# Kernel optimization log

Measured on AMD Instinct MI355X. Metric: run time of the kernel, lower is better.

The kernel has to match this reference:

```python
import jax, jax.numpy as jnp
import numpy as np

D_MODEL = 1024
NUM_HEADS = 16
HEAD_DIM = D_MODEL // NUM_HEADS


def setup_inputs() -> dict:
    key = jax.random.key(0)
    ks = jax.random.split(key, 9)
    s = 1.0 / np.sqrt(D_MODEL)
    x = jax.random.normal(ks[0], (2, 2048, D_MODEL), dtype=jnp.float32)
    Wq = jax.random.normal(ks[1], (D_MODEL, D_MODEL), dtype=jnp.float32) * s
    bq = jnp.zeros((D_MODEL,), dtype=jnp.float32)
    Wk = jax.random.normal(ks[2], (D_MODEL, D_MODEL), dtype=jnp.float32) * s
    bk = jnp.zeros((D_MODEL,), dtype=jnp.float32)
    Wv = jax.random.normal(ks[3], (D_MODEL, D_MODEL), dtype=jnp.float32) * s
    bv = jnp.zeros((D_MODEL,), dtype=jnp.float32)
    Wo = jax.random.normal(ks[4], (D_MODEL, D_MODEL), dtype=jnp.float32) * s
    bo = jnp.zeros((D_MODEL,), dtype=jnp.float32)
    return {"x": x, "Wq": Wq, "bq": bq, "Wk": Wk, "bk": bk,
            "Wv": Wv, "bv": bv, "Wo": Wo, "bo": bo}


def reference(x, Wq, bq, Wk, bk, Wv, bv, Wo, bo):
    B, S, D = x.shape
    H, Hd = NUM_HEADS, HEAD_DIM
    scale = 1.0 / np.sqrt(Hd)

    def split_heads(t):  # [B,S,D] -> [B,H,S,Hd]
        return t.reshape(B, S, H, Hd).transpose(0, 2, 1, 3)

    q = split_heads(x @ Wq + bq)
    k = split_heads(x @ Wk + bk)
    v = split_heads(x @ Wv + bv)

    scores = jnp.einsum('bhqd,bhkd->bhqk', q, k) * scale
    scores = scores - jnp.max(scores, axis=-1, keepdims=True)
    attn = jax.nn.softmax(scores, axis=-1)
    attended = jnp.einsum('bhqk,bhkd->bhqd', attn, v)
    attended = attended.transpose(0, 2, 1, 3).reshape(B, S, D)
    return attended @ Wo + bo
```

## Files before the change

kernel.cpp:

```cpp
#include <hip/hip_runtime.h>
#include <hip/hip_bf16.h>

typedef __bf16 bf16_t;
typedef __bf16 bf16x8 __attribute__((ext_vector_type(8)));
typedef __bf16 bf16x4 __attribute__((ext_vector_type(4)));
typedef float floatx4 __attribute__((ext_vector_type(4)));
typedef short short4v __attribute__((ext_vector_type(4)));

#define D_MODEL 1024
#define SEQ     2048
#define BATCH   2
#define NHEAD   16
#define HDIM    64
#define MTOT    (BATCH * SEQ)

#define QSCALE  0.18033688011112042f

union PBu { bf16x4 b; short4v s; };

__device__ __forceinline__ void async_copy16(const bf16_t* g, bf16_t* l) {
    __builtin_amdgcn_global_load_lds(
        (const __attribute__((address_space(1))) void*)g,
        (__attribute__((address_space(3))) void*)l, 16, 0, 0);
}

__global__ void cvt_f32_bf16(const float* __restrict__ x, bf16_t* __restrict__ y, int n) {
    int i = (blockIdx.x * 256 + threadIdx.x) * 4;
    if (i < n) {
        const float4 v = *(const float4*)(x + i);
        bf16x4 o = { (bf16_t)v.x, (bf16_t)v.y, (bf16_t)v.z, (bf16_t)v.w };
        *(bf16x4*)(y + i) = o;
    }
}

__global__ void transpose_w4(
    const float* __restrict__ W0, const float* __restrict__ W1,
    const float* __restrict__ W2, const float* __restrict__ W3,
    bf16_t* __restrict__ T0, bf16_t* __restrict__ T1,
    bf16_t* __restrict__ T2, bf16_t* __restrict__ T3)
{
    __shared__ float tile[32][33];
    const int z = blockIdx.z;
    const float* W = (z == 0) ? W0 : (z == 1) ? W1 : (z == 2) ? W2 : W3;
    bf16_t*     Wt = (z == 0) ? T0 : (z == 1) ? T1 : (z == 2) ? T2 : T3;
    const int tx = threadIdx.x, ty = threadIdx.y;
    const int k0 = blockIdx.y * 32, n0 = blockIdx.x * 32;
#pragma unroll
    for (int j = 0; j < 32; j += 8)
        tile[ty + j][tx] = W[(size_t)(k0 + ty + j) * D_MODEL + n0 + tx];
    __syncthreads();
#pragma unroll
    for (int j = 0; j < 32; j += 8)
        Wt[(size_t)(n0 + ty + j) * D_MODEL + k0 + tx] = (bf16_t)tile[tx][ty + j];
}

__device__ __forceinline__ void gemm_mainloop(
    const bf16_t* __restrict__ A, const bf16_t* __restrict__ Bt,
    int m0, int n0, bf16_t* As, bf16_t* Bs, floatx4 acc[4][4])
{
    const int tid  = threadIdx.x;
    const int lane = tid & 63;
    const int wid  = tid >> 6;
    const int quad = lane >> 4;
    const int col  = lane & 15;
    const int wm   = (wid >> 1) * 64;
    const int wn   = (wid & 1) * 64;
    const int srow = tid >> 3;
    const int scc  = ((tid & 7) ^ (srow & 7)) * 8;
    const int xorc = col & 7;

    const bf16_t* Ag = A  + (size_t)(m0 + srow) * D_MODEL + scc;
    const bf16_t* Bg = Bt + (size_t)(n0 + srow) * D_MODEL + scc;
    bf16_t* Al = As + tid * 8;
    bf16_t* Bl = Bs + tid * 8;

    for (int kb = 0; kb < D_MODEL; kb += 64) {
#pragma unroll
        for (int p = 0; p < 4; ++p) {
            async_copy16(Ag + kb + p * (32 * D_MODEL), Al + p * 2048);
            async_copy16(Bg + kb + p * (32 * D_MODEL), Bl + p * 2048);
        }
        __syncthreads();
#pragma unroll
        for (int kh = 0; kh < 2; ++kh) {
            bf16x8 af[4], bfr[4];
#pragma unroll
            for (int i = 0; i < 4; ++i)
                af[i] = *(const bf16x8*)(As + (wm + i * 16 + col) * 64 + (((kh * 4 + quad) ^ xorc) * 8));
#pragma unroll
            for (int j = 0; j < 4; ++j)
                bfr[j] = *(const bf16x8*)(Bs + (wn + j * 16 + col) * 64 + (((kh * 4 + quad) ^ xorc) * 8));
#pragma unroll
            for (int i = 0; i < 4; ++i)
#pragma unroll
                for (int j = 0; j < 4; ++j)
                    acc[i][j] = __builtin_amdgcn_mfma_f32_16x16x32_bf16(af[i], bfr[j], acc[i][j], 0, 0, 0);
        }
        __syncthreads();
    }
}

__global__ __launch_bounds__(256, 3) void gemm_qkv(
    const bf16_t* __restrict__ xb,
    const bf16_t* __restrict__ Wtq, const bf16_t* __restrict__ Wtk, const bf16_t* __restrict__ Wtv,
    const float* __restrict__ bq, const float* __restrict__ bk, const float* __restrict__ bv,
    bf16_t* __restrict__ Q, bf16_t* __restrict__ Kh, bf16_t* __restrict__ Vt)
{
    __shared__ bf16_t As[128 * 64];
    __shared__ bf16_t Bs[128 * 64];
    const int z = blockIdx.z;
    const bf16_t* Bt   = (z == 0) ? Wtq : (z == 1) ? Wtk : Wtv;
    const float*  bias = (z == 0) ? bq  : (z == 1) ? bk  : bv;
    bf16_t*       O    = (z == 0) ? Q   : (z == 1) ? Kh  : Vt;
    const float   qs   = (z == 0) ? QSCALE : 1.0f;
    const int m0 = blockIdx.y * 128;
    const int n0 = blockIdx.x * 128;

    floatx4 acc[4][4];
#pragma unroll
    for (int i = 0; i < 4; ++i)
#pragma unroll
        for (int j = 0; j < 4; ++j)
            acc[i][j] = (floatx4){0.f, 0.f, 0.f, 0.f};

    gemm_mainloop(xb, Bt, m0, n0, As, Bs, acc);

    const int tid  = threadIdx.x;
    const int lane = tid & 63;
    const int wid  = tid >> 6;
    const int quad = lane >> 4;
    const int col  = lane & 15;
    const int wm   = (wid >> 1) * 64;
    const int wn   = (wid & 1) * 64;

    if (z == 2) {
#pragma unroll
        for (int i = 0; i < 4; ++i) {
#pragma unroll
            for (int j = 0; j < 4; ++j) {
                const int n = n0 + wn + j * 16 + col;
                const float bb = bias[n];
                const int mb = m0 + wm + i * 16 + quad * 4;
                const size_t bhb = (size_t)((mb >> 11) * NHEAD + (n >> 6)) * (SEQ * HDIM);
                bf16x4 pk = { (bf16_t)(acc[i][j][0] + bb), (bf16_t)(acc[i][j][1] + bb),
                              (bf16_t)(acc[i][j][2] + bb), (bf16_t)(acc[i][j][3] + bb) };
                *(bf16x4*)(O + bhb + (size_t)(n & 63) * SEQ + (mb & 2047)) = pk;
            }
        }
    } else {
#pragma unroll
        for (int i = 0; i < 4; ++i) {
#pragma unroll
            for (int j = 0; j < 4; ++j) {
                const int n = n0 + wn + j * 16 + col;
                const float bb = bias[n];
#pragma unroll
                for (int r = 0; r < 4; ++r) {
                    const int m = m0 + wm + i * 16 + quad * 4 + r;
                    const float v = (acc[i][j][r] + bb) * qs;
                    const size_t bhb = (size_t)((m >> 11) * NHEAD + (n >> 6)) * (SEQ * HDIM);
                    O[bhb + (size_t)(m & 2047) * HDIM + (n & 63)] = (bf16_t)v;
                }
            }
        }
    }
}

__global__ __launch_bounds__(256, 2) void attn_kernel(
    const bf16_t* __restrict__ Q, const bf16_t* __restrict__ K,
    const bf16_t* __restrict__ Vt, bf16_t* __restrict__ A2)
{
    __shared__ bf16_t Ks[3][64 * 64];
    __shared__ bf16_t Vs[3][64 * 64];

    const int tid  = threadIdx.x;
    const int lane = tid & 63;
    const int wid  = tid >> 6;
    const int quad = lane >> 4;
    const int col  = lane & 15;
    const int xorc = col & 7;

    const int blk = blockIdx.x;
    const int idx = blk >> 3;
    const int bh  = (blk & 7) * 4 + (idx >> 4);
    const int q0  = (idx & 15) * 128;
    const int b   = bh >> 4, h = bh & 15;

    const bf16_t* Qb = Q  + (size_t)bh * (SEQ * HDIM);
    const bf16_t* Kb = K  + (size_t)bh * (SEQ * HDIM);
    const bf16_t* Vb = Vt + (size_t)bh * (SEQ * HDIM);

    bf16x8 qf[2][2];
#pragma unroll
    for (int g = 0; g < 2; ++g) {
        const int qrow = q0 + wid * 32 + g * 16 + col;
        qf[g][0] = *(const bf16x8*)(Qb + (size_t)qrow * HDIM + quad * 8);
        qf[g][1] = *(const bf16x8*)(Qb + (size_t)qrow * HDIM + 32 + quad * 8);
    }

    floatx4 o_acc[2][4];
    float lsum[2] = {0.f, 0.f};
#pragma unroll
    for (int g = 0; g < 2; ++g)
#pragma unroll
        for (int dt = 0; dt < 4; ++dt)
            o_acc[g][dt] = (floatx4){0.f, 0.f, 0.f, 0.f};

    const int srow = tid >> 3;
    const int scc  = ((tid & 7) ^ (srow & 7)) * 8;
    const bf16_t* Kg = Kb + (size_t)srow * HDIM + scc;
    const bf16_t* Vg = Vb + (size_t)srow * SEQ + scc;

    auto stage = [&](int ko, bf16_t* dk, bf16_t* dv) {
        async_copy16(Kg + (size_t)ko * HDIM, dk + tid * 8);
        async_copy16(Kg + (size_t)(ko + 32) * HDIM, dk + tid * 8 + 2048);
        async_copy16(Vg + ko, dv + tid * 8);
        async_copy16(Vg + (size_t)32 * SEQ + ko, dv + tid * 8 + 2048);
    };

    auto step = [&](const bf16_t* KsC, const bf16_t* VsC) {
        bf16x8 kf[4][2];
#pragma unroll
        for (int t = 0; t < 4; ++t) {
            kf[t][0] = *(const bf16x8*)(KsC + (t * 16 + col) * 64 + ((quad ^ xorc) * 8));
            kf[t][1] = *(const bf16x8*)(KsC + (t * 16 + col) * 64 + (((4 + quad) ^ xorc) * 8));
        }
        short4v vfr[4][4];
#pragma unroll
        for (int dt = 0; dt < 4; ++dt)
#pragma unroll
            for (int t = 0; t < 4; ++t) {
                const int sch = t * 2 + (quad >> 1);
                vfr[dt][t] = *(const short4v*)(VsC + (dt * 16 + col) * 64 + ((sch ^ xorc) * 8) + (quad & 1) * 4);
            }
#pragma unroll
        for (int g = 0; g < 2; ++g) {
            floatx4 s_acc[4];
            short4v pb[4];
            __builtin_amdgcn_s_setprio(1);
#pragma unroll
            for (int t = 0; t < 4; ++t) {
                s_acc[t] = (floatx4){0.f, 0.f, 0.f, 0.f};
                s_acc[t] = __builtin_amdgcn_mfma_f32_16x16x32_bf16(kf[t][0], qf[g][0], s_acc[t], 0, 0, 0);
                s_acc[t] = __builtin_amdgcn_mfma_f32_16x16x32_bf16(kf[t][1], qf[g][1], s_acc[t], 0, 0, 0);
            }
            __builtin_amdgcn_s_setprio(0);
            float ls = 0.f;
#pragma unroll
            for (int t = 0; t < 4; ++t) {
                const float p0 = __builtin_amdgcn_exp2f(s_acc[t][0]);
                const float p1 = __builtin_amdgcn_exp2f(s_acc[t][1]);
                const float p2 = __builtin_amdgcn_exp2f(s_acc[t][2]);
                const float p3 = __builtin_amdgcn_exp2f(s_acc[t][3]);
                ls += (p0 + p1) + (p2 + p3);
                PBu u;
                u.b = (bf16x4){ (bf16_t)p0, (bf16_t)p1, (bf16_t)p2, (bf16_t)p3 };
                pb[t] = u.s;
            }
            lsum[g] += ls;
            __builtin_amdgcn_s_setprio(1);
#pragma unroll
            for (int dt = 0; dt < 4; ++dt)
#pragma unroll
                for (int t = 0; t < 4; ++t)
                    o_acc[g][dt] = __builtin_amdgcn_mfma_f32_16x16x16bf16_1k(vfr[dt][t], pb[t], o_acc[g][dt], 0, 0, 0);
            __builtin_amdgcn_s_setprio(0);
        }
    };

    stage(0,  &Ks[0][0], &Vs[0][0]);
    stage(64, &Ks[1][0], &Vs[1][0]);

    bf16_t *k0 = &Ks[0][0], *k1 = &Ks[1][0], *k2 = &Ks[2][0];
    bf16_t *v0 = &Vs[0][0], *v1 = &Vs[1][0], *v2 = &Vs[2][0];

#pragma unroll 1
    for (int it = 0; it < 30; ++it) {
        asm volatile("s_waitcnt vmcnt(4)" ::: "memory");
        asm volatile("s_waitcnt lgkmcnt(0)" ::: "memory");
        __builtin_amdgcn_s_barrier();
        stage((it + 2) * 64, k2, v2);
        step(k0, v0);
        bf16_t* tk = k0; k0 = k1; k1 = k2; k2 = tk;
        bf16_t* tv = v0; v0 = v1; v1 = v2; v2 = tv;
    }
    asm volatile("s_waitcnt vmcnt(4)" ::: "memory");
    asm volatile("s_waitcnt lgkmcnt(0)" ::: "memory");
    __builtin_amdgcn_s_barrier();
    step(k0, v0);
    asm volatile("s_waitcnt vmcnt(0)" ::: "memory");
    asm volatile("s_waitcnt lgkmcnt(0)" ::: "memory");
    __builtin_amdgcn_s_barrier();
    step(k1, v1);

#pragma unroll
    for (int g = 0; g < 2; ++g) {
        float l = lsum[g];
        l += __shfl_xor(l, 16, 64);
        l += __shfl_xor(l, 32, 64);
        const float inv = 1.0f / l;
        const int qrow = q0 + wid * 32 + g * 16 + col;
        bf16_t* dst = A2 + ((size_t)(b * SEQ + qrow)) * D_MODEL + h * HDIM + quad * 4;
#pragma unroll
        for (int dt = 0; dt < 4; ++dt) {
            bf16x4 pk = { (bf16_t)(o_acc[g][dt][0] * inv), (bf16_t)(o_acc[g][dt][1] * inv),
                          (bf16_t)(o_acc[g][dt][2] * inv), (bf16_t)(o_acc[g][dt][3] * inv) };
            *(bf16x4*)(dst + dt * 16) = pk;
        }
    }
}

__global__ __launch_bounds__(256, 3) void gemm_proj(
    const bf16_t* __restrict__ A2, const bf16_t* __restrict__ Wto,
    const float* __restrict__ bo, float* __restrict__ out)
{
    __shared__ bf16_t As[64 * 64];
    __shared__ bf16_t Bs[128 * 64];
    const int m0 = blockIdx.y * 64;
    const int n0 = blockIdx.x * 128;

    const int tid  = threadIdx.x;
    const int lane = tid & 63;
    const int wid  = tid >> 6;
    const int quad = lane >> 4;
    const int col  = lane & 15;
    const int wm   = (wid >> 1) * 32;
    const int wn   = (wid & 1) * 64;
    const int srow = tid >> 3;
    const int scc  = ((tid & 7) ^ (srow & 7)) * 8;
    const int xorc = col & 7;

    floatx4 acc[2][4];
#pragma unroll
    for (int i = 0; i < 2; ++i)
#pragma unroll
        for (int j = 0; j < 4; ++j)
            acc[i][j] = (floatx4){0.f, 0.f, 0.f, 0.f};

    const bf16_t* Ag = A2  + (size_t)(m0 + srow) * D_MODEL + scc;
    const bf16_t* Bg = Wto + (size_t)(n0 + srow) * D_MODEL + scc;
    bf16_t* Al = As + tid * 8;
    bf16_t* Bl = Bs + tid * 8;

    for (int kb = 0; kb < D_MODEL; kb += 64) {
#pragma unroll
        for (int p = 0; p < 2; ++p)
            async_copy16(Ag + kb + p * (32 * D_MODEL), Al + p * 2048);
#pragma unroll
        for (int p = 0; p < 4; ++p)
            async_copy16(Bg + kb + p * (32 * D_MODEL), Bl + p * 2048);
        __syncthreads();
#pragma unroll
        for (int kh = 0; kh < 2; ++kh) {
            bf16x8 af[2], bfr[4];
#pragma unroll
            for (int i = 0; i < 2; ++i)
                af[i] = *(const bf16x8*)(As + (wm + i * 16 + col) * 64 + (((kh * 4 + quad) ^ xorc) * 8));
#pragma unroll
            for (int j = 0; j < 4; ++j)
                bfr[j] = *(const bf16x8*)(Bs + (wn + j * 16 + col) * 64 + (((kh * 4 + quad) ^ xorc) * 8));
#pragma unroll
            for (int i = 0; i < 2; ++i)
#pragma unroll
                for (int j = 0; j < 4; ++j)
                    acc[i][j] = __builtin_amdgcn_mfma_f32_16x16x32_bf16(af[i], bfr[j], acc[i][j], 0, 0, 0);
        }
        __syncthreads();
    }

#pragma unroll
    for (int i = 0; i < 2; ++i) {
#pragma unroll
        for (int j = 0; j < 4; ++j) {
            const int n = n0 + wn + j * 16 + col;
            const float bb = bo[n];
#pragma unroll
            for (int r = 0; r < 4; ++r) {
                const int m = m0 + wm + i * 16 + quad * 4 + r;
                out[(size_t)m * D_MODEL + n] = acc[i][j][r] + bb;
            }
        }
    }
}

extern "C" void kernel_launch(void* const* d_in, const int* in_sizes, int n_in,
                              void* d_out, int out_size, void* d_ws, size_t ws_size,
                              hipStream_t stream) {
    const float* x  = (const float*)d_in[0];
    const float* Wq = (const float*)d_in[1];
    const float* bq = (const float*)d_in[2];
    const float* Wk = (const float*)d_in[3];
    const float* bk = (const float*)d_in[4];
    const float* Wv = (const float*)d_in[5];
    const float* bv = (const float*)d_in[6];
    const float* Wo = (const float*)d_in[7];
    const float* bo = (const float*)d_in[8];
    float* out = (float*)d_out;

    const size_t MB = 1ull << 20;
    char* ws = (char*)d_ws;
    bf16_t* Q     = (bf16_t*)(ws + 0 * MB);
    bf16_t* Kh    = (bf16_t*)(ws + 8 * MB);
    bf16_t* Vt    = (bf16_t*)(ws + 16 * MB);
    bf16_t* A2    = (bf16_t*)(ws + 24 * MB);
    bf16_t* xb    = (bf16_t*)(ws + 32 * MB);
    bf16_t* Wtq   = (bf16_t*)(ws + 40 * MB);
    bf16_t* Wtk   = (bf16_t*)(ws + 42 * MB);
    bf16_t* Wtv   = (bf16_t*)(ws + 44 * MB);
    bf16_t* Wto   = (bf16_t*)(ws + 46 * MB);

    const int nx = MTOT * D_MODEL;
    cvt_f32_bf16<<<nx / (256 * 4), 256, 0, stream>>>(x, xb, nx);

    transpose_w4<<<dim3(D_MODEL / 32, D_MODEL / 32, 4), dim3(32, 8), 0, stream>>>(
        Wq, Wk, Wv, Wo, Wtq, Wtk, Wtv, Wto);

    gemm_qkv<<<dim3(D_MODEL / 128, MTOT / 128, 3), 256, 0, stream>>>(
        xb, Wtq, Wtk, Wtv, bq, bk, bv, Q, Kh, Vt);

    attn_kernel<<<dim3(512), 256, 0, stream>>>(Q, Kh, Vt, A2);

    gemm_proj<<<dim3(D_MODEL / 128, MTOT / 64), 256, 0, stream>>>(A2, Wto, bo, out);
}
```

Baseline: 186.0 us.

## Split attention KV tiles across warp pairs and double-buffer LDS with reduction epilogue

Reorganises the attention kernel so each warp handles 64 query rows but only half of each 64-key tile (split-K across warp pairs). This halves per-warp K/V fragment LDS reads per query, since each K/V fragment is now reused across four query groups. It also moves from triple to double buffering and adds an LDS reduction of partial outputs and row sums at the end. LDS is shared through a union with the reduction buffer. The changes add register pressure (o_acc doubles to 64 floats) and an extra barrier per tile, and the smaller prefetch depth may expose load latency.

```diff
diff --git a/kernel.cpp b/kernel.cpp
--- a/kernel.cpp
+++ b/kernel.cpp
@@ -170,8 +170,10 @@
     const bf16_t* __restrict__ Q, const bf16_t* __restrict__ K,
     const bf16_t* __restrict__ Vt, bf16_t* __restrict__ A2)
 {
-    __shared__ bf16_t Ks[3][64 * 64];
-    __shared__ bf16_t Vs[3][64 * 64];
+    __shared__ union SM {
+        struct { bf16_t Ks[2][64 * 64]; bf16_t Vs[2][64 * 64]; } t;
+        struct { float Ored[2][64 * 68]; float Lred[2][64]; } r;
+    } sm;
 
     const int tid  = threadIdx.x;
     const int lane = tid & 63;
@@ -179,6 +181,8 @@
     const int quad = lane >> 4;
     const int col  = lane & 15;
     const int xorc = col & 7;
+    const int qh   = wid & 1;
+    const int kh   = wid >> 1;
 
     const int blk = blockIdx.x;
     const int idx = blk >> 3;
@@ -190,18 +194,18 @@
     const bf16_t* Kb = K  + (size_t)bh * (SEQ * HDIM);
     const bf16_t* Vb = Vt + (size_t)bh * (SEQ * HDIM);
 
-    bf16x8 qf[2][2];
-#pragma unroll
-    for (int g = 0; g < 2; ++g) {
-        const int qrow = q0 + wid * 32 + g * 16 + col;
+    bf16x8 qf[4][2];
+#pragma unroll
+    for (int g = 0; g < 4; ++g) {
+        const int qrow = q0 + qh * 64 + g * 16 + col;
         qf[g][0] = *(const bf16x8*)(Qb + (size_t)qrow * HDIM + quad * 8);
         qf[g][1] = *(const bf16x8*)(Qb + (size_t)qrow * HDIM + 32 + quad * 8);
     }
 
-    floatx4 o_acc[2][4];
-    float lsum[2] = {0.f, 0.f};
-#pragma unroll
-    for (int g = 0; g < 2; ++g)
+    floatx4 o_acc[4][4];
+    float lsum[4] = {0.f, 0.f, 0.f, 0.f};
+#pragma unroll
+    for (int g = 0; g < 4; ++g)
 #pragma unroll
         for (int dt = 0; dt < 4; ++dt)
             o_acc[g][dt] = (floatx4){0.f, 0.f, 0.f, 0.f};
@@ -210,6 +214,10 @@
     const int scc  = ((tid & 7) ^ (srow & 7)) * 8;
     const bf16_t* Kg = Kb + (size_t)srow * HDIM + scc;
     const bf16_t* Vg = Vb + (size_t)srow * SEQ + scc;
+    bf16_t* Ks0 = &sm.t.Ks[0][0];
+    bf16_t* Ks1 = &sm.t.Ks[1][0];
+    bf16_t* Vs0 = &sm.t.Vs[0][0];
+    bf16_t* Vs1 = &sm.t.Vs[1][0];
 
     auto stage = [&](int ko, bf16_t* dk, bf16_t* dv) {
         async_copy16(Kg + (size_t)ko * HDIM, dk + tid * 8);
@@ -219,93 +227,121 @@
     };
 
     auto step = [&](const bf16_t* KsC, const bf16_t* VsC) {
-        bf16x8 kf[4][2];
-#pragma unroll
-        for (int t = 0; t < 4; ++t) {
-            kf[t][0] = *(const bf16x8*)(KsC + (t * 16 + col) * 64 + ((quad ^ xorc) * 8));
-            kf[t][1] = *(const bf16x8*)(KsC + (t * 16 + col) * 64 + (((4 + quad) ^ xorc) * 8));
-        }
-        short4v vfr[4][4];
+        bf16x8 kf[2][2];
+#pragma unroll
+        for (int tt = 0; tt < 2; ++tt) {
+            const int t = kh * 2 + tt;
+            kf[tt][0] = *(const bf16x8*)(KsC + (t * 16 + col) * 64 + ((quad ^ xorc) * 8));
+            kf[tt][1] = *(const bf16x8*)(KsC + (t * 16 + col) * 64 + (((4 + quad) ^ xorc) * 8));
+        }
+        short4v vfr[4][2];
 #pragma unroll
         for (int dt = 0; dt < 4; ++dt)
 #pragma unroll
-            for (int t = 0; t < 4; ++t) {
+            for (int tt = 0; tt < 2; ++tt) {
+                const int t = kh * 2 + tt;
                 const int sch = t * 2 + (quad >> 1);
-                vfr[dt][t] = *(const short4v*)(VsC + (dt * 16 + col) * 64 + ((sch ^ xorc) * 8) + (quad & 1) * 4);
-            }
-#pragma unroll
-        for (int g = 0; g < 2; ++g) {
-            floatx4 s_acc[4];
-            short4v pb[4];
+                vfr[dt][tt] = *(const short4v*)(VsC + (dt * 16 + col) * 64 + ((sch ^ xorc) * 8) + (quad & 1) * 4);
+            }
+#pragma unroll
+        for (int g = 0; g < 4; ++g) {
+            floatx4 s_acc[2];
+            short4v pb[2];
             __builtin_amdgcn_s_setprio(1);
 #pragma unroll
-            for (int t = 0; t < 4; ++t) {
-                s_acc[t] = (floatx4){0.f, 0.f, 0.f, 0.f};
-                s_acc[t] = __builtin_amdgcn_mfma_f32_16x16x32_bf16(kf[t][0], qf[g][0], s_acc[t], 0, 0, 0);
-                s_acc[t] = __builtin_amdgcn_mfma_f32_16x16x32_bf16(kf[t][1], qf[g][1], s_acc[t], 0, 0, 0);
+            for (int tt = 0; tt < 2; ++tt) {
+                s_acc[tt] = (floatx4){0.f, 0.f, 0.f, 0.f};
+                s_acc[tt] = __builtin_amdgcn_mfma_f32_16x16x32_bf16(kf[tt][0], qf[g][0], s_acc[tt], 0, 0, 0);
+                s_acc[tt] = __builtin_amdgcn_mfma_f32_16x16x32_bf16(kf[tt][1], qf[g][1], s_acc[tt], 0, 0, 0);
             }
             __builtin_amdgcn_s_setprio(0);
             float ls = 0.f;
 #pragma unroll
-            for (int t = 0; t < 4; ++t) {
-                const float p0 = __builtin_amdgcn_exp2f(s_acc[t][0]);
-                const float p1 = __builtin_amdgcn_exp2f(s_acc[t][1]);
-                const float p2 = __builtin_amdgcn_exp2f(s_acc[t][2]);
-                const float p3 = __builtin_amdgcn_exp2f(s_acc[t][3]);
+            for (int tt = 0; tt < 2; ++tt) {
+                const float p0 = __builtin_amdgcn_exp2f(s_acc[tt][0]);
+                const float p1 = __builtin_amdgcn_exp2f(s_acc[tt][1]);
+                const float p2 = __builtin_amdgcn_exp2f(s_acc[tt][2]);
+                const float p3 = __builtin_amdgcn_exp2f(s_acc[tt][3]);
                 ls += (p0 + p1) + (p2 + p3);
                 PBu u;
                 u.b = (bf16x4){ (bf16_t)p0, (bf16_t)p1, (bf16_t)p2, (bf16_t)p3 };
-                pb[t] = u.s;
+                pb[tt] = u.s;
             }
             lsum[g] += ls;
             __builtin_amdgcn_s_setprio(1);
 #pragma unroll
             for (int dt = 0; dt < 4; ++dt)
 #pragma unroll
-                for (int t = 0; t < 4; ++t)
-                    o_acc[g][dt] = __builtin_amdgcn_mfma_f32_16x16x16bf16_1k(vfr[dt][t], pb[t], o_acc[g][dt], 0, 0, 0);
+                for (int tt = 0; tt < 2; ++tt)
+                    o_acc[g][dt] = __builtin_amdgcn_mfma_f32_16x16x16bf16_1k(vfr[dt][tt], pb[tt], o_acc[g][dt], 0, 0, 0);
             __builtin_amdgcn_s_setprio(0);
         }
     };
 
-    stage(0,  &Ks[0][0], &Vs[0][0]);
-    stage(64, &Ks[1][0], &Vs[1][0]);
-
-    bf16_t *k0 = &Ks[0][0], *k1 = &Ks[1][0], *k2 = &Ks[2][0];
-    bf16_t *v0 = &Vs[0][0], *v1 = &Vs[1][0], *v2 = &Vs[2][0];
+    stage(0,  Ks0, Vs0);
+    stage(64, Ks1, Vs1);
 
 #pragma unroll 1
-    for (int it = 0; it < 30; ++it) {
+    for (int it2 = 0; it2 < 15; ++it2) {
         asm volatile("s_waitcnt vmcnt(4)" ::: "memory");
+        __builtin_amdgcn_s_barrier();
+        step(Ks0, Vs0);
         asm volatile("s_waitcnt lgkmcnt(0)" ::: "memory");
         __builtin_amdgcn_s_barrier();
-        stage((it + 2) * 64, k2, v2);
-        step(k0, v0);
-        bf16_t* tk = k0; k0 = k1; k1 = k2; k2 = tk;
-        bf16_t* tv = v0; v0 = v1; v1 = v2; v2 = tv;
+        stage((2 * it2 + 2) * 64, Ks0, Vs0);
+
+        asm volatile("s_waitcnt vmcnt(4)" ::: "memory");
+        __builtin_amdgcn_s_barrier();
+        step(Ks1, Vs1);
+        asm volatile("s_waitcnt lgkmcnt(0)" ::: "memory");
+        __builtin_amdgcn_s_barrier();
+        stage((2 * it2 + 3) * 64, Ks1, Vs1);
     }
     asm volatile("s_waitcnt vmcnt(4)" ::: "memory");
-    asm volatile("s_waitcnt lgkmcnt(0)" ::: "memory");
     __builtin_amdgcn_s_barrier();
-    step(k0, v0);
+    step(Ks0, Vs0);
     asm volatile("s_waitcnt vmcnt(0)" ::: "memory");
-    asm volatile("s_waitcnt lgkmcnt(0)" ::: "memory");
     __builtin_amdgcn_s_barrier();
-    step(k1, v1);
-
-#pragma unroll
-    for (int g = 0; g < 2; ++g) {
-        float l = lsum[g];
-        l += __shfl_xor(l, 16, 64);
-        l += __shfl_xor(l, 32, 64);
-        const float inv = 1.0f / l;
-        const int qrow = q0 + wid * 32 + g * 16 + col;
-        bf16_t* dst = A2 + ((size_t)(b * SEQ + qrow)) * D_MODEL + h * HDIM + quad * 4;
-#pragma unroll
-        for (int dt = 0; dt < 4; ++dt) {
-            bf16x4 pk = { (bf16_t)(o_acc[g][dt][0] * inv), (bf16_t)(o_acc[g][dt][1] * inv),
-                          (bf16_t)(o_acc[g][dt][2] * inv), (bf16_t)(o_acc[g][dt][3] * inv) };
-            *(bf16x4*)(dst + dt * 16) = pk;
+    step(Ks1, Vs1);
+
+#pragma unroll
+    for (int g = 0; g < 4; ++g) {
+        lsum[g] += __shfl_xor(lsum[g], 16, 64);
+        lsum[g] += __shfl_xor(lsum[g], 32, 64);
+    }
+    __syncthreads();
+    if (kh == 1) {
+#pragma unroll
+        for (int g = 0; g < 4; ++g) {
+#pragma unroll
+            for (int dt = 0; dt < 4; ++dt)
+#pragma unroll
+                for (int r = 0; r < 4; ++r) {
+                    const int d = dt * 16 + quad * 4 + r;
+                    sm.r.Ored[qh][d * 68 + g * 16 + col] = o_acc[g][dt][r];
+                }
+            if (quad == 0)
+                sm.r.Lred[qh][g * 16 + col] = lsum[g];
+        }
+    }
+    __syncthreads();
+    if (kh == 0) {
+#pragma unroll
+        for (int g = 0; g < 4; ++g) {
+            const float l = lsum[g] + sm.r.Lred[qh][g * 16 + col];
+            const float inv = 1.0f / l;
+            const int qrow = q0 + qh * 64 + g * 16 + col;
+            bf16_t* dst = A2 + ((size_t)(b * SEQ + qrow)) * D_MODEL + h * HDIM + quad * 4;
+#pragma unroll
+            for (int dt = 0; dt < 4; ++dt) {
+                bf16x4 pk;
+#pragma unroll
+                for (int r = 0; r < 4; ++r) {
+                    const int d = dt * 16 + quad * 4 + r;
+                    pk[r] = (bf16_t)((o_acc[g][dt][r] + sm.r.Ored[qh][d * 68 + g * 16 + col]) * inv);
+                }
+                *(bf16x4*)(dst + dt * 16) = pk;
+            }
         }
     }
 }
```

Result: no change. 188.9 us (+1.5%).
